# Kernel tuning notes

Measured on AMD Instinct MI355X. Metric: run time of the kernel, lower is better.

Reference implementation:

```python
import jax, jax.numpy as jnp
import numpy as np

B, L, D_MODEL, HEAD = 8, 2048, 1024, 64

def setup_inputs() -> dict:
    key = jax.random.key(0)
    ks = jax.random.split(key, 6)
    idx_k = jax.random.normal(ks[0], (B, L, D_MODEL), dtype=jnp.float32)
    idx_q = jax.random.normal(ks[1], (B, L, D_MODEL), dtype=jnp.float32)
    idx_v = jax.random.normal(ks[2], (B, L, D_MODEL), dtype=jnp.float32)
    # causal lower-triangular mask, broadcast over batch
    msk = jnp.tril(jnp.ones((L, L), dtype=jnp.int32))
    s = 1.0 / np.sqrt(D_MODEL)
    Wk = jax.random.uniform(ks[3], (D_MODEL, HEAD), jnp.float32, -s, s)
    Wq = jax.random.uniform(ks[4], (D_MODEL, HEAD), jnp.float32, -s, s)
    Wv = jax.random.uniform(ks[5], (D_MODEL, HEAD), jnp.float32, -s, s)
    return {"idx_k": idx_k, "idx_q": idx_q, "idx_v": idx_v, "msk": msk,
            "Wk": Wk, "Wq": Wq, "Wv": Wv}

def reference(idx_k, idx_q, idx_v, msk, Wk, Wq, Wv):
    # projections (Linear, no bias): [B,L,d_model] @ [d_model,head] -> [B,L,head]
    K = idx_k @ Wk
    Q = idx_q @ Wq
    V = idx_v @ Wv
    scale = K.shape[-1] ** -0.5
    # scores: [B,Lq,Lk]
    S = jnp.einsum('bqh,bkh->bqk', Q, K) * scale
    S = jnp.where(msk == 0, jnp.float32(-1e9), S)
    att = jax.nn.softmax(S, axis=-1)  # dropout=0.0 (inference)
    out = jnp.einsum('bqk,bkh->bqh', att, V)
    return out
```

## Files before the change

kernel.cpp:

```cpp
#include <hip/hip_runtime.h>

typedef __bf16 bf16x8 __attribute__((ext_vector_type(8)));
typedef float f32x4 __attribute__((ext_vector_type(4)));
typedef unsigned short u16;

#define LSEQ 2048
#define DMODEL 1024
#define HEADD 64
#define NBATCH 8

__device__ __forceinline__ u16 cvt(float f) {
  __bf16 h = (__bf16)f;
  return __builtin_bit_cast(u16, h);
}

#define BARRIER_LGKM() do {                                   \
    asm volatile("s_waitcnt lgkmcnt(0)" ::: "memory");        \
    __builtin_amdgcn_sched_barrier(0);                        \
    __builtin_amdgcn_s_barrier();                             \
    __builtin_amdgcn_sched_barrier(0);                        \
  } while (0)

__global__ __launch_bounds__(256) void wt_kernel(
    const float* __restrict__ Wk, const float* __restrict__ Wq,
    const float* __restrict__ Wv, u16* __restrict__ wp) {
  int idx = blockIdx.x * 256 + threadIdx.x;
  int j = idx & 7;
  int lane = (idx >> 3) & 63;
  int ks = (idx >> 9) & 31;
  int c = (idx >> 14) & 3;
  int p = idx >> 16;
  const float* W = (p == 0) ? Wk : ((p == 1) ? Wq : Wv);
  int k = ks * 32 + 8 * (lane >> 4) + j;
  int col = 16 * c + (lane & 15);
  wp[idx] = cvt(W[(size_t)k * HEADD + col]);
}

__global__ __launch_bounds__(128) void proj_kernel(
    const float* __restrict__ ik, const float* __restrict__ iq, const float* __restrict__ iv,
    const u16* __restrict__ wp, u16* __restrict__ Kb, u16* __restrict__ Qb,
    u16* __restrict__ Vt) {
  __shared__ __align__(16) u16 Asw[2][16 * 128];
  int p = blockIdx.y;
  const float* A = (p == 0) ? ik : ((p == 1) ? iq : iv);
  const u16* Wp = wp + (size_t)p * 4 * 32 * 512;
  int t = threadIdx.x;
  int lane = t & 63;
  int wv = t >> 6;
  int l15 = lane & 15, g = lane >> 4;
  int rowbase = blockIdx.x * 16;
  const float* srcbase = A + (size_t)rowbase * DMODEL;

  int srow0 = t >> 5;
  int scol = (t & 31) * 4;

  float4 stgA[4], stgB[4];
  bf16x8 wfr[4][2];

  auto issue = [&](float4 (&stg)[4], int kc) {
#pragma unroll
    for (int i = 0; i < 4; ++i)
      stg[i] = *(const float4*)(srcbase + (size_t)(i * 4 + srow0) * DMODEL + kc + scol);
  };
  auto commit = [&](const float4 (&stg)[4], u16* basep) {
    char* base = (char*)basep;
#pragma unroll
    for (int i = 0; i < 4; ++i) {
      int row = i * 4 + srow0;
      ushort4 pk;
      pk.x = cvt(stg[i].x); pk.y = cvt(stg[i].y);
      pk.z = cvt(stg[i].z); pk.w = cvt(stg[i].w);
      int byte = row * 256 + ((scol * 2) ^ ((row & 7) << 4));
      *(ushort4*)(base + byte) = pk;
    }
  };
  auto wload = [&](int c8) {
#pragma unroll
    for (int ks = 0; ks < 4; ++ks)
#pragma unroll
      for (int cc = 0; cc < 2; ++cc)
        wfr[ks][cc] = *(const bf16x8*)(
            Wp + ((size_t)(wv * 2 + cc) * 32 + c8 * 4 + ks) * 512 + lane * 8);
  };

  f32x4 acc[2] = {};
  int abase = l15 * 256;
  int aswz = (l15 & 7) << 4;

  auto computeC = [&](const char* lbase) {
#pragma unroll
    for (int ks = 0; ks < 4; ++ks) {
      bf16x8 af = *(const bf16x8*)(lbase + abase + ((ks * 64 + 16 * g) ^ aswz));
#pragma unroll
      for (int cc = 0; cc < 2; ++cc)
        acc[cc] = __builtin_amdgcn_mfma_f32_16x16x32_bf16(af, wfr[ks][cc], acc[cc], 0, 0, 0);
    }
  };

  issue(stgA, 0);
  issue(stgB, 128);
  commit(stgA, &Asw[0][0]);
  BARRIER_LGKM();

#pragma unroll 1
  for (int cc8 = 0; cc8 < 8; cc8 += 2) {
    wload(cc8);
    __builtin_amdgcn_sched_barrier(0);
    if (cc8 < 6) issue(stgA, (cc8 + 2) * 128);
    __builtin_amdgcn_sched_barrier(0);
    computeC((const char*)&Asw[0][0]);
    commit(stgB, &Asw[1][0]);
    BARRIER_LGKM();
    wload(cc8 + 1);
    __builtin_amdgcn_sched_barrier(0);
    if (cc8 < 5) issue(stgB, (cc8 + 3) * 128);
    __builtin_amdgcn_sched_barrier(0);
    computeC((const char*)&Asw[1][0]);
    if (cc8 < 6) commit(stgA, &Asw[0][0]);
    BARRIER_LGKM();
  }

  if (p == 2) {
    int row0 = rowbase + 4 * g;
    int b = row0 >> 11, tok = row0 & 2047;
#pragma unroll
    for (int cc = 0; cc < 2; ++cc) {
      int d = 16 * (wv * 2 + cc) + l15;
      ushort4 pk;
      pk.x = cvt(acc[cc][0]); pk.y = cvt(acc[cc][1]);
      pk.z = cvt(acc[cc][2]); pk.w = cvt(acc[cc][3]);
      *(ushort4*)(Vt + ((size_t)b * HEADD + d) * LSEQ + tok) = pk;
    }
  } else {
    u16* dst = (p == 0) ? Kb : Qb;
    float s = (p == 1) ? 0.125f : 1.0f;
#pragma unroll
    for (int cc = 0; cc < 2; ++cc)
#pragma unroll
      for (int r = 0; r < 4; ++r)
        dst[(size_t)(rowbase + 4 * g + r) * HEADD + 16 * (wv * 2 + cc) + l15] =
            cvt(acc[cc][r] * s);
  }
}

__global__ __launch_bounds__(128) void attn_kernel(
    const u16* __restrict__ Kb, const u16* __restrict__ Qb, const u16* __restrict__ Vt,
    float* __restrict__ out) {
  __shared__ __align__(16) u16 plds[2][16 * 40];
  __shared__ __align__(16) float mrg[64][18];
  int lane = threadIdx.x & 63;
  int wv = threadIdx.x >> 6;
  int l15 = lane & 15, g = lane >> 4;
  int id = blockIdx.x;
  int b = id & 7;
  int qt = 127 - (id >> 3);
  int qbase = qt * 16;

  const u16* Qp = Qb + ((size_t)b * LSEQ + qbase) * HEADD;
  const u16* Kp = Kb + (size_t)b * LSEQ * HEADD;
  const u16* Vp = Vt + (size_t)b * HEADD * LSEQ;

  bf16x8 qf[2];
#pragma unroll
  for (int ds = 0; ds < 2; ++ds)
    qf[ds] = *(const bf16x8*)(Qp + (size_t)l15 * HEADD + 32 * ds + 8 * g);

  f32x4 acc[4] = {};
  float m = -1e30f, lsum = 0.f;
  int q_abs = qbase + l15;
  int ntiles = (qbase + 47) >> 5;

  for (int t = wv; t < ntiles; t += 2) {
    int kbase = t * 32;
    f32x4 sacc[2] = {};
#pragma unroll
    for (int f = 0; f < 2; ++f)
#pragma unroll
      for (int ds = 0; ds < 2; ++ds) {
        bf16x8 kf = *(const bf16x8*)(Kp + (size_t)(kbase + 16 * f + l15) * HEADD + 32 * ds + 8 * g);
        sacc[f] = __builtin_amdgcn_mfma_f32_16x16x32_bf16(kf, qf[ds], sacc[f], 0, 0, 0);
      }

    float sv[2][4];
    float tmax = -1e30f;
#pragma unroll
    for (int f = 0; f < 2; ++f)
#pragma unroll
      for (int r = 0; r < 4; ++r) {
        int key = kbase + 16 * f + 4 * g + r;
        float s = (key <= q_abs) ? sacc[f][r] : -1e30f;
        sv[f][r] = s;
        tmax = fmaxf(tmax, s);
      }
    tmax = fmaxf(tmax, __shfl_xor(tmax, 16));
    tmax = fmaxf(tmax, __shfl_xor(tmax, 32));
    float mnew = fmaxf(m, tmax);
    float al = __expf(m - mnew);
    float pv[2][4];
    float rs = 0.f;
#pragma unroll
    for (int f = 0; f < 2; ++f)
#pragma unroll
      for (int r = 0; r < 4; ++r) {
        pv[f][r] = __expf(sv[f][r] - mnew);
        rs += pv[f][r];
      }
    rs += __shfl_xor(rs, 16);
    rs += __shfl_xor(rs, 32);
    lsum = lsum * al + rs;
    m = mnew;

    float alr[4];
#pragma unroll
    for (int r = 0; r < 4; ++r) alr[r] = __shfl(al, 4 * g + r);
#pragma unroll
    for (int c = 0; c < 4; ++c)
#pragma unroll
      for (int r = 0; r < 4; ++r) acc[c][r] *= alr[r];

#pragma unroll
    for (int f = 0; f < 2; ++f) {
      ushort4 pk;
      pk.x = cvt(pv[f][0]); pk.y = cvt(pv[f][1]);
      pk.z = cvt(pv[f][2]); pk.w = cvt(pv[f][3]);
      *(ushort4*)&plds[wv][l15 * 40 + 16 * f + 4 * g] = pk;
    }
    bf16x8 ap = *(const bf16x8*)&plds[wv][l15 * 40 + 8 * g];

#pragma unroll
    for (int c = 0; c < 4; ++c) {
      bf16x8 vf = *(const bf16x8*)(Vp + (size_t)(16 * c + l15) * LSEQ + kbase + 8 * g);
      acc[c] = __builtin_amdgcn_mfma_f32_16x16x32_bf16(ap, vf, acc[c], 0, 0, 0);
    }
  }

  if (wv == 1) {
#pragma unroll
    for (int c = 0; c < 4; ++c)
#pragma unroll
      for (int r = 0; r < 4; ++r) mrg[lane][c * 4 + r] = acc[c][r];
    mrg[lane][16] = m;
    mrg[lane][17] = lsum;
  }
  __syncthreads();
  if (wv == 0) {
    float m1 = mrg[lane][16], l1 = mrg[lane][17];
    float mT = fmaxf(m, m1);
    float e0 = __expf(m - mT), e1 = __expf(m1 - mT);
    float lT = lsum * e0 + l1 * e1;
    float e0r[4], e1r[4], li[4];
#pragma unroll
    for (int r = 0; r < 4; ++r) {
      e0r[r] = __shfl(e0, 4 * g + r);
      e1r[r] = __shfl(e1, 4 * g + r);
      li[r] = 1.0f / __shfl(lT, 4 * g + r);
    }
#pragma unroll
    for (int c = 0; c < 4; ++c)
#pragma unroll
      for (int r = 0; r < 4; ++r) {
        float v = acc[c][r] * e0r[r] + mrg[lane][c * 4 + r] * e1r[r];
        out[((size_t)b * LSEQ + qbase + 4 * g + r) * HEADD + 16 * c + l15] = v * li[r];
      }
  }
}

extern "C" void kernel_launch(void* const* d_in, const int* in_sizes, int n_in,
                              void* d_out, int out_size, void* d_ws, size_t ws_size,
                              hipStream_t stream) {
  const float* idx_k = (const float*)d_in[0];
  const float* idx_q = (const float*)d_in[1];
  const float* idx_v = (const float*)d_in[2];
  const float* Wk = (const float*)d_in[4];
  const float* Wq = (const float*)d_in[5];
  const float* Wv = (const float*)d_in[6];
  float* out = (float*)d_out;

  char* ws = (char*)d_ws;
  const size_t WT_BYTES = (size_t)3 * 4 * 32 * 512 * 2;
  const size_t MAT_BYTES = (size_t)NBATCH * LSEQ * HEADD * 2;
  u16* wp = (u16*)ws;
  u16* Kb = (u16*)(ws + WT_BYTES);
  u16* Qb = (u16*)(ws + WT_BYTES + MAT_BYTES);
  u16* Vt = (u16*)(ws + WT_BYTES + 2 * MAT_BYTES);

  hipLaunchKernelGGL(wt_kernel, dim3(768), dim3(256), 0, stream, Wk, Wq, Wv, wp);
  hipLaunchKernelGGL(proj_kernel, dim3(1024, 3), dim3(128), 0, stream,
                     idx_k, idx_q, idx_v, wp, Kb, Qb, Vt);
  hipLaunchKernelGGL(attn_kernel, dim3(1024), dim3(128), 0, stream, Kb, Qb, Vt, out);
}
```

Baseline: 86.25 us.

## Split projection into single-wave blocks with XCD-aware tile mapping, drop barriers

The projection kernel now uses one 64-thread wave per block, each computing a 16-row tile for half of the head columns, with twice as many blocks. Because each block is a single wave, the double-buffered shared memory and the s_barrier synchronisation are replaced by a single LDS buffer written and read in program order. Block indices are remapped so that the two half-column blocks for the same rows land on the same XCD, so the second read of the fp32 input rows is meant to be served from L2. The aim is more independent waves and no block-wide stalls, at the cost of fetching every input row twice.

```diff
diff --git a/kernel.cpp b/kernel.cpp
--- a/kernel.cpp
+++ b/kernel.cpp
@@ -13,13 +13,6 @@
   __bf16 h = (__bf16)f;
   return __builtin_bit_cast(u16, h);
 }
-
-#define BARRIER_LGKM() do {                                   \
-    asm volatile("s_waitcnt lgkmcnt(0)" ::: "memory");        \
-    __builtin_amdgcn_sched_barrier(0);                        \
-    __builtin_amdgcn_s_barrier();                             \
-    __builtin_amdgcn_sched_barrier(0);                        \
-  } while (0)
 
 __global__ __launch_bounds__(256) void wt_kernel(
     const float* __restrict__ Wk, const float* __restrict__ Wq,
@@ -36,88 +29,79 @@
   wp[idx] = cvt(W[(size_t)k * HEADD + col]);
 }
 
-__global__ __launch_bounds__(128) void proj_kernel(
+__global__ __launch_bounds__(64, 6) void proj_kernel(
     const float* __restrict__ ik, const float* __restrict__ iq, const float* __restrict__ iv,
     const u16* __restrict__ wp, u16* __restrict__ Kb, u16* __restrict__ Qb,
     u16* __restrict__ Vt) {
-  __shared__ __align__(16) u16 Asw[2][16 * 128];
+  __shared__ __align__(16) u16 As[16 * 64];
   int p = blockIdx.y;
   const float* A = (p == 0) ? ik : ((p == 1) ? iq : iv);
   const u16* Wp = wp + (size_t)p * 4 * 32 * 512;
-  int t = threadIdx.x;
-  int lane = t & 63;
-  int wv = t >> 6;
+  int x = blockIdx.x;
+  int xcd = x & 7;
+  int idx = x >> 3;
+  int h = idx & 1;
+  int rt = (idx >> 1) * 8 + xcd;
+  int lane = threadIdx.x;
   int l15 = lane & 15, g = lane >> 4;
-  int rowbase = blockIdx.x * 16;
+  int rowbase = rt * 16;
   const float* srcbase = A + (size_t)rowbase * DMODEL;
 
-  int srow0 = t >> 5;
-  int scol = (t & 31) * 4;
+  int srow = g;
+  int sf4 = l15;
 
   float4 stgA[4], stgB[4];
-  bf16x8 wfr[4][2];
+  bf16x8 wfr[2][2];
 
   auto issue = [&](float4 (&stg)[4], int kc) {
 #pragma unroll
     for (int i = 0; i < 4; ++i)
-      stg[i] = *(const float4*)(srcbase + (size_t)(i * 4 + srow0) * DMODEL + kc + scol);
-  };
-  auto commit = [&](const float4 (&stg)[4], u16* basep) {
-    char* base = (char*)basep;
+      stg[i] = *(const float4*)(srcbase + (size_t)(i * 4 + srow) * DMODEL + kc + sf4 * 4);
+  };
+  auto commit = [&](const float4 (&stg)[4]) {
+    char* base = (char*)As;
 #pragma unroll
     for (int i = 0; i < 4; ++i) {
-      int row = i * 4 + srow0;
+      int row = i * 4 + srow;
       ushort4 pk;
       pk.x = cvt(stg[i].x); pk.y = cvt(stg[i].y);
       pk.z = cvt(stg[i].z); pk.w = cvt(stg[i].w);
-      int byte = row * 256 + ((scol * 2) ^ ((row & 7) << 4));
+      int byte = row * 128 + ((sf4 * 8) ^ ((row & 7) << 4));
       *(ushort4*)(base + byte) = pk;
     }
   };
-  auto wload = [&](int c8) {
-#pragma unroll
-    for (int ks = 0; ks < 4; ++ks)
+  auto wload = [&](int c16) {
+#pragma unroll
+    for (int ks2 = 0; ks2 < 2; ++ks2)
 #pragma unroll
       for (int cc = 0; cc < 2; ++cc)
-        wfr[ks][cc] = *(const bf16x8*)(
-            Wp + ((size_t)(wv * 2 + cc) * 32 + c8 * 4 + ks) * 512 + lane * 8);
+        wfr[ks2][cc] = *(const bf16x8*)(
+            Wp + ((size_t)(h * 2 + cc) * 32 + c16 * 2 + ks2) * 512 + lane * 8);
   };
 
   f32x4 acc[2] = {};
-  int abase = l15 * 256;
   int aswz = (l15 & 7) << 4;
-
-  auto computeC = [&](const char* lbase) {
-#pragma unroll
-    for (int ks = 0; ks < 4; ++ks) {
-      bf16x8 af = *(const bf16x8*)(lbase + abase + ((ks * 64 + 16 * g) ^ aswz));
+  auto computeC = [&]() {
+#pragma unroll
+    for (int ks2 = 0; ks2 < 2; ++ks2) {
+      bf16x8 af = *(const bf16x8*)((const char*)As + l15 * 128 + ((ks2 * 64 + 16 * g) ^ aswz));
 #pragma unroll
       for (int cc = 0; cc < 2; ++cc)
-        acc[cc] = __builtin_amdgcn_mfma_f32_16x16x32_bf16(af, wfr[ks][cc], acc[cc], 0, 0, 0);
+        acc[cc] = __builtin_amdgcn_mfma_f32_16x16x32_bf16(af, wfr[ks2][cc], acc[cc], 0, 0, 0);
     }
   };
 
   issue(stgA, 0);
-  issue(stgB, 128);
-  commit(stgA, &Asw[0][0]);
-  BARRIER_LGKM();
-
 #pragma unroll 1
-  for (int cc8 = 0; cc8 < 8; cc8 += 2) {
-    wload(cc8);
-    __builtin_amdgcn_sched_barrier(0);
-    if (cc8 < 6) issue(stgA, (cc8 + 2) * 128);
-    __builtin_amdgcn_sched_barrier(0);
-    computeC((const char*)&Asw[0][0]);
-    commit(stgB, &Asw[1][0]);
-    BARRIER_LGKM();
-    wload(cc8 + 1);
-    __builtin_amdgcn_sched_barrier(0);
-    if (cc8 < 5) issue(stgB, (cc8 + 3) * 128);
-    __builtin_amdgcn_sched_barrier(0);
-    computeC((const char*)&Asw[1][0]);
-    if (cc8 < 6) commit(stgA, &Asw[0][0]);
-    BARRIER_LGKM();
+  for (int c = 0; c < 16; c += 2) {
+    wload(c);
+    if (c < 15) issue(stgB, (c + 1) * 64);
+    commit(stgA);
+    computeC();
+    wload(c + 1);
+    if (c < 14) issue(stgA, (c + 2) * 64);
+    commit(stgB);
+    computeC();
   }
 
   if (p == 2) {
@@ -125,7 +109,7 @@
     int b = row0 >> 11, tok = row0 & 2047;
 #pragma unroll
     for (int cc = 0; cc < 2; ++cc) {
-      int d = 16 * (wv * 2 + cc) + l15;
+      int d = 16 * (2 * h + cc) + l15;
       ushort4 pk;
       pk.x = cvt(acc[cc][0]); pk.y = cvt(acc[cc][1]);
       pk.z = cvt(acc[cc][2]); pk.w = cvt(acc[cc][3]);
@@ -138,7 +122,7 @@
     for (int cc = 0; cc < 2; ++cc)
 #pragma unroll
       for (int r = 0; r < 4; ++r)
-        dst[(size_t)(rowbase + 4 * g + r) * HEADD + 16 * (wv * 2 + cc) + l15] =
+        dst[(size_t)(rowbase + 4 * g + r) * HEADD + 16 * (2 * h + cc) + l15] =
             cvt(acc[cc][r] * s);
   }
 }
@@ -285,7 +269,7 @@
   u16* Vt = (u16*)(ws + WT_BYTES + 2 * MAT_BYTES);
 
   hipLaunchKernelGGL(wt_kernel, dim3(768), dim3(256), 0, stream, Wk, Wq, Wv, wp);
-  hipLaunchKernelGGL(proj_kernel, dim3(1024, 3), dim3(128), 0, stream,
+  hipLaunchKernelGGL(proj_kernel, dim3(2048, 3), dim3(64), 0, stream,
                      idx_k, idx_q, idx_v, wp, Kb, Qb, Vt);
   hipLaunchKernelGGL(attn_kernel, dim3(1024), dim3(128), 0, stream, Kb, Qb, Vt, out);
 }
```

After: 87.02 us. Within noise of the previous version (+0.9%).
